# Kernel tuning notes

Measured on AMD Instinct MI355X. Metric: run time of the kernel, lower is better.

Reference implementation:

```python
import jax, jax.numpy as jnp
import numpy as np

N = 100000      # nodes
E = 1600000     # edges (avg degree 16)
IN = 128
OUT = 256


def setup_inputs() -> dict:
    key = jax.random.key(0)
    ks = jax.random.split(key, 8)
    x = jax.random.normal(ks[0], (N, IN), dtype=jnp.float32)
    edge_index = jax.random.randint(ks[1], (2, E), 0, N, dtype=jnp.int64)
    # GCNConv weights (glorot-ish scale) and biases
    W1 = jax.random.normal(ks[2], (IN, OUT), dtype=jnp.float32) / np.float32(np.sqrt(IN))
    b1 = jnp.zeros((OUT,), jnp.float32)
    W2 = jax.random.normal(ks[3], (OUT, OUT), dtype=jnp.float32) / np.float32(np.sqrt(OUT))
    b2 = jnp.zeros((OUT,), jnp.float32)
    # projection Linear(IN, OUT)
    Wp = jax.random.normal(ks[4], (IN, OUT), dtype=jnp.float32) / np.float32(np.sqrt(IN))
    bp = jax.random.normal(ks[5], (OUT,), dtype=jnp.float32) * 0.01
    return {"x": x, "edge_index": edge_index, "W1": W1, "b1": b1,
            "W2": W2, "b2": b2, "Wp": Wp, "bp": bp}


def _gcn_conv(x, W, b, src, dst, n):
    """PyG GCNConv: D^{-1/2}(A+I)D^{-1/2} X W + b. src/dst already include self-loops."""
    xw = x @ W                                              # [n, out]
    ones = jnp.ones(src.shape[0], dtype=xw.dtype)
    deg = jax.ops.segment_sum(ones, dst, num_segments=n)    # in-degree incl. self-loop
    dinv = jnp.where(deg > 0, jax.lax.rsqrt(deg), 0.0)
    norm = dinv[src] * dinv[dst]                            # [e]
    msgs = xw[src] * norm[:, None]                          # gather + scale
    out = jax.ops.segment_sum(msgs, dst, num_segments=n)    # scatter-add
    return out + b


def reference(x, edge_index, W1, b1, W2, b2, Wp, bp):
    n = x.shape[0]
    loop = jnp.arange(n, dtype=edge_index.dtype)            # self-loops
    src = jnp.concatenate([edge_index[0], loop])
    dst = jnp.concatenate([edge_index[1], loop])
    out = jax.nn.relu(_gcn_conv(x, W1, b1, src, dst, n))
    out = _gcn_conv(out, W2, b2, src, dst, n)
    identity = x @ Wp + bp                                  # projection (IN != OUT)
    return jax.nn.relu(out + identity)
```

## Files before the change

kernel.cpp:

```cpp
#include <hip/hip_runtime.h>

#define NODES 100000
#define EDGES 1600000
#define FIN   128
#define FOUT  256
#define NBUCK 196

typedef __bf16 bf16;
typedef __bf16 bf16x8 __attribute__((ext_vector_type(8)));
typedef __bf16 bf16x4 __attribute__((ext_vector_type(4)));
typedef __bf16 bf16x2 __attribute__((ext_vector_type(2)));
typedef float  f32x4  __attribute__((ext_vector_type(4)));
typedef float  f32x2  __attribute__((ext_vector_type(2)));

__device__ __forceinline__ f32x2 bf2f(unsigned w) {
    f32x2 r;
    r[0] = __uint_as_float(w << 16);
    r[1] = __uint_as_float(w & 0xffff0000u);
    return r;
}

__device__ __forceinline__ void acc_u4(f32x2 a[4], uint4 w) {
    a[0] += bf2f(w.x); a[1] += bf2f(w.y);
    a[2] += bf2f(w.z); a[3] += bf2f(w.w);
}

__global__ __launch_bounds__(256) void detect_kernel(const void* __restrict__ x,
                                                     const int* __restrict__ ei,
                                                     int* __restrict__ flags) {
    __shared__ int s_f32_evidence;
    __shared__ int s_odd_nonzero;
    int t = threadIdx.x;
    if (t == 0) { s_f32_evidence = 0; s_odd_nonzero = 0; }
    __syncthreads();
    const bf16* xb = (const bf16*)x;
    int local_f32 = 0;
    for (int i = t; i < 4096; i += 256) {
        float v = fabsf((float)xb[i]);
        if (!(v < 1e4f)) local_f32 = 1;
    }
    if (local_f32) atomicOr(&s_f32_evidence, 1);
    int local_odd = 0;
    for (int k = t; k < 1024; k += 256) {
        if (ei[2 * k + 1] != 0) local_odd = 1;
    }
    if (local_odd) atomicOr(&s_odd_nonzero, 1);
    __syncthreads();
    if (t == 0) {
        flags[0] = s_f32_evidence ? 0 : 1;
        flags[1] = s_odd_nonzero ? 0 : 1;
    }
}

__device__ __forceinline__ int edge_at(const int* __restrict__ ei, int which, int i,
                                       int is64) {
    if (is64) return ei[2 * (which * EDGES + i)];
    return ei[which * EDGES + i];
}

__global__ __launch_bounds__(512) void deg_count(const int* __restrict__ ei,
                                                 int* __restrict__ deg,
                                                 int* __restrict__ bhist,
                                                 const int* __restrict__ flags) {
    __shared__ int lh[256];
    int t = threadIdx.x;
    if (t < 256) lh[t] = 0;
    __syncthreads();
    int i = blockIdx.x * 512 + t;
    if (i < EDGES) {
        int is64 = flags[1];
        int s = edge_at(ei, 0, i, is64);
        int d = edge_at(ei, 1, i, is64);
        if (s >= 0 && s < NODES && d >= 0 && d < NODES) {
            atomicAdd(&deg[d], 1);
            atomicAdd(&lh[d >> 9], 1);
        }
    }
    __syncthreads();
    if (t < NBUCK && lh[t] > 0) atomicAdd(&bhist[t], lh[t]);
}

__global__ __launch_bounds__(1024) void scan1(const int* __restrict__ deg,
                                              int* __restrict__ col_ptr,
                                              int* __restrict__ blksum, int n) {
    __shared__ int sm[1024];
    int t = threadIdx.x;
    int i = blockIdx.x * 1024 + t;
    int v = (i < n) ? deg[i] + 1 : 0;
    sm[t] = v;
    __syncthreads();
    for (int off = 1; off < 1024; off <<= 1) {
        int u = (t >= off) ? sm[t - off] : 0;
        __syncthreads();
        sm[t] += u;
        __syncthreads();
    }
    if (i <= n) col_ptr[i] = sm[t] - v;
    if (t == 1023) blksum[blockIdx.x] = sm[t];
}

__global__ __launch_bounds__(128) void scan2(int* blk, int nblk) {
    __shared__ int sm[128];
    int t = threadIdx.x;
    int v = (t < nblk) ? blk[t] : 0;
    sm[t] = v;
    __syncthreads();
    for (int off = 1; off < 128; off <<= 1) {
        int u = (t >= off) ? sm[t - off] : 0;
        __syncthreads();
        sm[t] += u;
        __syncthreads();
    }
    if (t < nblk) blk[t] = sm[t] - v;
}

__global__ __launch_bounds__(256) void scan3(int* __restrict__ col_ptr,
                                             const int* __restrict__ blkoff,
                                             const int* __restrict__ deg,
                                             float* __restrict__ dinv,
                                             int* __restrict__ col_idx, int n) {
    int i = blockIdx.x * 256 + threadIdx.x;
    if (i <= n) {
        int v = col_ptr[i] + blkoff[i >> 10];
        col_ptr[i] = v;
        if (i < n) col_idx[v] = i;
    }
    if (i < n) dinv[i] = rsqrtf((float)deg[i] + 1.0f);
}

__global__ __launch_bounds__(256) void bucket_scan(const int* __restrict__ bhist,
                                                   int* __restrict__ bbase,
                                                   int* __restrict__ bcur) {
    __shared__ int sm[256];
    int t = threadIdx.x;
    int v = (t < NBUCK) ? bhist[t] : 0;
    sm[t] = v;
    __syncthreads();
    for (int off = 1; off < 256; off <<= 1) {
        int u = (t >= off) ? sm[t - off] : 0;
        __syncthreads();
        sm[t] += u;
        __syncthreads();
    }
    if (t < NBUCK) {
        int ex = sm[t] - v;
        bbase[t] = ex;
        bcur[t]  = ex;
        if (t == NBUCK - 1) bbase[NBUCK] = sm[t];
    }
}

#define EPB 4096
__global__ __launch_bounds__(256) void partition_edges(const int* __restrict__ ei,
                                                       int* __restrict__ bcur,
                                                       uint2* __restrict__ pairs,
                                                       const int* __restrict__ flags) {
    __shared__ int lh[256], sc[256], lst[256], lcu[256], gb[256];
    __shared__ uint2 stage[EPB];
    int t = threadIdx.x;
    int base = blockIdx.x * EPB;
    int is64 = flags[1];

    lh[t] = 0;
    __syncthreads();

    int es[16], ed[16];
#pragma unroll
    for (int j = 0; j < 16; ++j) {
        int i = base + j * 256 + t;
        int s = -1, d = -1;
        if (i < EDGES) {
            s = edge_at(ei, 0, i, is64);
            d = edge_at(ei, 1, i, is64);
            if (s < 0 || s >= NODES || d < 0 || d >= NODES) d = -1;
        }
        es[j] = s; ed[j] = d;
        if (d >= 0) atomicAdd(&lh[d >> 9], 1);
    }
    __syncthreads();
    sc[t] = lh[t];
    __syncthreads();
    for (int off = 1; off < 256; off <<= 1) {
        int u = (t >= off) ? sc[t - off] : 0;
        __syncthreads();
        sc[t] += u;
        __syncthreads();
    }
    int start = sc[t] - lh[t];
    lst[t] = start;
    lcu[t] = start;
    __syncthreads();
#pragma unroll
    for (int j = 0; j < 16; ++j) {
        if (ed[j] >= 0) {
            int p = atomicAdd(&lcu[ed[j] >> 9], 1);
            stage[p] = make_uint2((unsigned)es[j], (unsigned)ed[j]);
        }
    }
    __syncthreads();
    if (t < NBUCK && lh[t] > 0) gb[t] = atomicAdd(&bcur[t], lh[t]);
    __syncthreads();
    int nval = sc[255];
    for (int slot = t; slot < nval; slot += 256) {
        uint2 e = stage[slot];
        int b = (int)(e.y >> 9);
        pairs[(size_t)gb[b] + (slot - lst[b])] = e;
    }
}

__global__ __launch_bounds__(512) void fine_fill(const uint2* __restrict__ pairs,
                                                 const int* __restrict__ bbase,
                                                 const int* __restrict__ col_ptr,
                                                 int* __restrict__ col_idx) {
    __shared__ int lcur[512];
    int b = blockIdx.x;
    int t = threadIdx.x;
    int node = (b << 9) + t;
    lcur[t] = (node < NODES) ? col_ptr[node] + 1 : 0;
    __syncthreads();
    int beg = bbase[b], end = bbase[b + 1];
    for (int i = beg + t; i < end; i += 512) {
        uint2 e = pairs[i];
        int pos = atomicAdd(&lcur[e.y & 511], 1);
        col_idx[pos] = (int)e.x;
    }
}

__global__ __launch_bounds__(256) void pack_all(const void* __restrict__ W1,
                                                const void* __restrict__ W2,
                                                const void* __restrict__ Wp,
                                                const void* __restrict__ b1,
                                                const void* __restrict__ b2,
                                                const void* __restrict__ bp,
                                                bf16* __restrict__ W1p, bf16* __restrict__ W2p,
                                                bf16* __restrict__ Wpp, bf16* __restrict__ b1b,
                                                bf16* __restrict__ b2b, bf16* __restrict__ bpb,
                                                const int* __restrict__ flags) {
    int fl = flags[0];
    int b = blockIdx.x;
    if (b < 512) {
        const void* W; bf16* Wo; int idx;
        if (b < 128)      { W = W1; Wo = W1p; idx = b * 256 + threadIdx.x; }
        else if (b < 384) { W = W2; Wo = W2p; idx = (b - 128) * 256 + threadIdx.x; }
        else              { W = Wp; Wo = Wpp; idx = (b - 384) * 256 + threadIdx.x; }
        int j    = idx & 7;
        int lane = (idx >> 3) & 63;
        int ct   = (idx >> 9) & 15;
        int kt   = idx >> 13;
        int k = kt * 32 + (lane >> 4) * 8 + j;
        int n = ct * 16 + (lane & 15);
        Wo[idx] = fl ? ((const bf16*)W)[k * 256 + n]
                     : (bf16)(((const float*)W)[k * 256 + n]);
    } else {
        const void* bb; bf16* bo;
        if (b == 512)      { bb = b1; bo = b1b; }
        else if (b == 513) { bb = b2; bo = b2b; }
        else               { bb = bp; bo = bpb; }
        int i = threadIdx.x;
        bo[i] = fl ? ((const bf16*)bb)[i] : (bf16)(((const float*)bb)[i]);
    }
}

__global__ __launch_bounds__(256) void scale_x(const void* __restrict__ xv,
                                               const float* __restrict__ dinv,
                                               bf16* __restrict__ Xs,
                                               const int* __restrict__ flags) {
    int idx = blockIdx.x * 256 + threadIdx.x;
    if (idx >= NODES * 16) return;
    int row = idx >> 4, seg = idx & 15;
    float di = dinv[row];
    bf16x8 o;
    if (flags[0]) {
        bf16x8 v = *(const bf16x8*)((const bf16*)xv + (size_t)row * FIN + seg * 8);
#pragma unroll
        for (int j = 0; j < 8; ++j) o[j] = (bf16)(di * (float)v[j]);
    } else {
        const float* p = (const float*)xv + (size_t)row * FIN + seg * 8;
        f32x4 lo = *(const f32x4*)p;
        f32x4 hi = *(const f32x4*)(p + 4);
#pragma unroll
        for (int j = 0; j < 4; ++j) { o[j] = (bf16)(di * lo[j]); o[j + 4] = (bf16)(di * hi[j]); }
    }
    *(bf16x8*)(Xs + (size_t)row * FIN + seg * 8) = o;
}

__global__ __launch_bounds__(256) void gemm_proj(const void* __restrict__ Av,
                                                 const bf16* __restrict__ Wpk,
                                                 const bf16* __restrict__ biasp,
                                                 const bf16* __restrict__ bias2,
                                                 bf16* __restrict__ projb,
                                                 const int* __restrict__ flags) {
    int a_f32 = (flags[0] == 0);
    int wave = threadIdx.x >> 6;
    int lane = threadIdx.x & 63;
    int row0 = blockIdx.x * 64;
    int lr = lane & 15;
    int lk = (lane >> 4) * 8;

    int arow[4];
#pragma unroll
    for (int rf = 0; rf < 4; ++rf) {
        int r = row0 + rf * 16 + lr;
        arow[rf] = r < NODES ? r : (NODES - 1);
    }

    f32x4 acc[4][4];
    f32x4 z = {0.f, 0.f, 0.f, 0.f};
#pragma unroll
    for (int i = 0; i < 4; ++i)
#pragma unroll
        for (int j = 0; j < 4; ++j) acc[i][j] = z;

    for (int kt = 0; kt < 4; ++kt) {
        bf16x8 af[4];
        if (!a_f32) {
            const bf16* Ab = (const bf16*)Av + kt * 32 + lk;
#pragma unroll
            for (int rf = 0; rf < 4; ++rf)
                af[rf] = *(const bf16x8*)(Ab + (size_t)arow[rf] * FIN);
        } else {
            const float* Af = (const float*)Av + kt * 32 + lk;
#pragma unroll
            for (int rf = 0; rf < 4; ++rf) {
                const float* p = Af + (size_t)arow[rf] * FIN;
                f32x4 lo = *(const f32x4*)p;
                f32x4 hi = *(const f32x4*)(p + 4);
                af[rf][0] = (bf16)lo[0]; af[rf][1] = (bf16)lo[1];
                af[rf][2] = (bf16)lo[2]; af[rf][3] = (bf16)lo[3];
                af[rf][4] = (bf16)hi[0]; af[rf][5] = (bf16)hi[1];
                af[rf][6] = (bf16)hi[2]; af[rf][7] = (bf16)hi[3];
            }
        }
        const bf16* wb = Wpk + ((size_t)(kt * 16 + wave * 4) * 64 + lane) * 8;
        bf16x8 bfv[4];
#pragma unroll
        for (int cf = 0; cf < 4; ++cf)
            bfv[cf] = *(const bf16x8*)(wb + cf * 512);
#pragma unroll
        for (int rf = 0; rf < 4; ++rf)
#pragma unroll
            for (int cf = 0; cf < 4; ++cf)
                acc[rf][cf] = __builtin_amdgcn_mfma_f32_16x16x32_bf16(
                    af[rf], bfv[cf], acc[rf][cf], 0, 0, 0);
    }

    int rb = (lane >> 4) * 4;
#pragma unroll
    for (int rf = 0; rf < 4; ++rf) {
#pragma unroll
        for (int r = 0; r < 4; ++r) {
            int row = row0 + rf * 16 + rb + r;
            if (row >= NODES) continue;
#pragma unroll
            for (int cf = 0; cf < 4; ++cf) {
                int col = wave * 64 + cf * 16 + lr;
                float v = acc[rf][cf][r] + (float)biasp[col] + (float)bias2[col];
                projb[(size_t)row * 256 + col] = (bf16)v;
            }
        }
    }
}

__global__ __launch_bounds__(256) void gemm_tile(const bf16* __restrict__ A,
                                                 const bf16* __restrict__ Wpk,
                                                 int K,
                                                 const float* __restrict__ dinv,
                                                 const bf16* __restrict__ bias,
                                                 int relu,
                                                 bf16* __restrict__ out) {
    int wave = threadIdx.x >> 6;
    int lane = threadIdx.x & 63;
    int row0 = blockIdx.x * 64;
    int lr = lane & 15;
    int lk = (lane >> 4) * 8;

    int arow[4];
#pragma unroll
    for (int rf = 0; rf < 4; ++rf) {
        int r = row0 + rf * 16 + lr;
        arow[rf] = r < NODES ? r : (NODES - 1);
    }

    f32x4 acc[4][4];
    f32x4 z = {0.f, 0.f, 0.f, 0.f};
#pragma unroll
    for (int i = 0; i < 4; ++i)
#pragma unroll
        for (int j = 0; j < 4; ++j) acc[i][j] = z;

    int ktiles = K >> 5;
    for (int kt = 0; kt < ktiles; ++kt) {
        const bf16* Ab = A + kt * 32 + lk;
        bf16x8 af[4];
#pragma unroll
        for (int rf = 0; rf < 4; ++rf)
            af[rf] = *(const bf16x8*)(Ab + (size_t)arow[rf] * K);
        const bf16* wb = Wpk + ((size_t)(kt * 16 + wave * 4) * 64 + lane) * 8;
        bf16x8 bfv[4];
#pragma unroll
        for (int cf = 0; cf < 4; ++cf)
            bfv[cf] = *(const bf16x8*)(wb + cf * 512);
#pragma unroll
        for (int rf = 0; rf < 4; ++rf)
#pragma unroll
            for (int cf = 0; cf < 4; ++cf)
                acc[rf][cf] = __builtin_amdgcn_mfma_f32_16x16x32_bf16(
                    af[rf], bfv[cf], acc[rf][cf], 0, 0, 0);
    }

    int rb = (lane >> 4) * 4;
#pragma unroll
    for (int rf = 0; rf < 4; ++rf) {
#pragma unroll
        for (int r = 0; r < 4; ++r) {
            int row = row0 + rf * 16 + rb + r;
            if (row >= NODES) continue;
            float s = dinv ? dinv[row] : 1.0f;
#pragma unroll
            for (int cf = 0; cf < 4; ++cf) {
                int col = wave * 64 + cf * 16 + lr;
                float v = acc[rf][cf][r] * s;
                if (bias) v += (float)bias[col];
                if (relu) v = fmaxf(v, 0.0f);
                out[(size_t)row * 256 + col] = (bf16)v;
            }
        }
    }
}

__device__ __forceinline__ float sel_reduce8(f32x2 acc2[4], int rg) {
    f32x2 a  = (rg & 4) ? acc2[2] : acc2[0];
    f32x2 b  = (rg & 4) ? acc2[3] : acc2[1];
    f32x2 sa = (rg & 4) ? acc2[0] : acc2[2];
    f32x2 sb = (rg & 4) ? acc2[1] : acc2[3];
    f32x2 t;
    t[0] = __shfl_xor(sa[0], 32); t[1] = __shfl_xor(sa[1], 32); a += t;
    t[0] = __shfl_xor(sb[0], 32); t[1] = __shfl_xor(sb[1], 32); b += t;
    f32x2 c = (rg & 2) ? b : a;
    f32x2 s = (rg & 2) ? a : b;
    t[0] = __shfl_xor(s[0], 16); t[1] = __shfl_xor(s[1], 16); c += t;
    float e  = (rg & 1) ? c[1] : c[0];
    float s2 = (rg & 1) ? c[0] : c[1];
    e += __shfl_xor(s2, 8);
    return e;
}

__device__ __forceinline__ f32x2 sel_reduce4(f32x2 a[4], int rg) {
    f32x2 k0 = (rg & 2) ? a[2] : a[0];
    f32x2 k1 = (rg & 2) ? a[3] : a[1];
    f32x2 s0 = (rg & 2) ? a[0] : a[2];
    f32x2 s1 = (rg & 2) ? a[1] : a[3];
    f32x2 t;
    t[0] = __shfl_xor(s0[0], 32); t[1] = __shfl_xor(s0[1], 32); k0 += t;
    t[0] = __shfl_xor(s1[0], 32); t[1] = __shfl_xor(s1[1], 32); k1 += t;
    f32x2 c = (rg & 1) ? k1 : k0;
    f32x2 s = (rg & 1) ? k0 : k1;
    t[0] = __shfl_xor(s[0], 16); t[1] = __shfl_xor(s[1], 16); c += t;
    return c;
}

__global__ __launch_bounds__(256) void gather1(const int* __restrict__ col_ptr,
                                               const int* __restrict__ col_idx,
                                               const bf16* __restrict__ Xs,
                                               const float* __restrict__ dinv,
                                               bf16* __restrict__ aggX) {
    int b = blockIdx.x;
    int slice = b & 1;
    int wave  = threadIdx.x >> 6;
    int wid   = (b >> 1) * 4 + wave;
    int lane  = threadIdx.x & 63;
    if (wid >= NODES) return;
    int beg = col_ptr[wid], end = col_ptr[wid + 1];
    int li = lane & 7;
    int rg = lane >> 3;
    int ch = slice * 64 + li * 8 + rg;
    float di = dinv[wid];

    const char* Xl = (const char*)Xs + slice * 128 + li * 16;
    f32x2 acc2[4];
#pragma unroll
    for (int d = 0; d < 4; ++d) { acc2[d][0] = 0.f; acc2[d][1] = 0.f; }
    for (int chunk = beg; chunk < end; chunk += 64) {
        int gpos = chunk + lane;
        int idx = -2;
        if (gpos < end) idx = col_idx[gpos];
        int moff = idx << 8;
        int cnt = end - chunk; if (cnt > 64) cnt = 64;
        int j = 0;
        for (; j + 16 <= cnt; j += 16) {
            int so0 = __shfl(moff, j + rg);
            int so1 = __shfl(moff, j + 8 + rg);
            uint4 w0 = *(const uint4*)(Xl + so0);
            uint4 w1 = *(const uint4*)(Xl + so1);
            acc_u4(acc2, w0); acc_u4(acc2, w1);
        }
        for (; j < cnt; j += 8) {
            int so = __shfl(moff, j + rg);
            uint4 w = *(const uint4*)(Xl + so);
            acc_u4(acc2, w);
        }
    }
    float aval = sel_reduce8(acc2, rg);
    aggX[(size_t)wid * FIN + ch] = (bf16)(di * aval);
}

__global__ __launch_bounds__(256) void gather2(const int* __restrict__ col_ptr,
                                               const int* __restrict__ col_idx,
                                               const bf16* __restrict__ Y2,
                                               const float* __restrict__ dinv,
                                               const bf16* __restrict__ projb,
                                               void* __restrict__ outv,
                                               const int* __restrict__ flags) {
    int io_f32 = (flags[0] == 0);
    int b = blockIdx.x;
    int slice = b & 1;
    int wave  = threadIdx.x >> 6;
    int wid   = (b >> 1) * 4 + wave;
    int lane  = threadIdx.x & 63;
    if (wid >= NODES) return;
    int beg = col_ptr[wid], end = col_ptr[wid + 1];
    int li = lane & 15;
    int rg = lane >> 4;
    int ch0 = slice * 128 + li * 8 + rg * 2;
    size_t obase = (size_t)wid * 256 + ch0;

    float di = dinv[wid];
    bf16x2 pjv = *(const bf16x2*)(projb + obase);

    const char* Yl = (const char*)Y2 + slice * 256 + li * 16;
    f32x2 acc2[4];
#pragma unroll
    for (int d = 0; d < 4; ++d) { acc2[d][0] = 0.f; acc2[d][1] = 0.f; }
    for (int chunk = beg; chunk < end; chunk += 64) {
        int gpos = chunk + lane;
        int idx = -2;
        if (gpos < end) idx = col_idx[gpos];
        int moff = idx << 9;
        int cnt = end - chunk; if (cnt > 64) cnt = 64;
        int j = 0;
        for (; j + 16 <= cnt; j += 16) {
            int so0 = __shfl(moff, j + rg);
            int so1 = __shfl(moff, j + 4 + rg);
            int so2 = __shfl(moff, j + 8 + rg);
            int so3 = __shfl(moff, j + 12 + rg);
            uint4 w0 = *(const uint4*)(Yl + so0);
            uint4 w1 = *(const uint4*)(Yl + so1);
            uint4 w2 = *(const uint4*)(Yl + so2);
            uint4 w3 = *(const uint4*)(Yl + so3);
            acc_u4(acc2, w0); acc_u4(acc2, w1);
            acc_u4(acc2, w2); acc_u4(acc2, w3);
        }
        for (; j < cnt; j += 4) {
            int so = __shfl(moff, j + rg);
            uint4 w = *(const uint4*)(Yl + so);
            acc_u4(acc2, w);
        }
    }
    f32x2 s = sel_reduce4(acc2, rg);
    float r0 = fmaxf(di * s[0] + (float)pjv[0], 0.0f);
    float r1 = fmaxf(di * s[1] + (float)pjv[1], 0.0f);

    if (io_f32) {
        f32x2 o; o[0] = r0; o[1] = r1;
        __builtin_nontemporal_store(o, (f32x2*)((float*)outv + obase));
    } else {
        bf16x2 o; o[0] = (bf16)r0; o[1] = (bf16)r1;
        __builtin_nontemporal_store(o, (bf16x2*)((bf16*)outv + obase));
    }
}

__global__ __launch_bounds__(256) void zero_out(bf16* out, int nelem) {
    int i = blockIdx.x * 256 + threadIdx.x;
    if (i < nelem) out[i] = (bf16)0.0f;
}

extern "C" void kernel_launch(void* const* d_in, const int* in_sizes, int n_in,
                              void* d_out, int out_size, void* d_ws, size_t ws_size,
                              hipStream_t stream) {
    const void* x   = d_in[0];
    const int*  ei  = (const int*)d_in[1];
    const void* W1  = d_in[2];
    const void* b1  = d_in[3];
    const void* W2  = d_in[4];
    const void* b2  = d_in[5];
    const void* Wp  = d_in[6];
    const void* bp  = d_in[7];

    const size_t CIDX_ALLOC = 6800384;
    const size_t NEEDED = 401408ull * 3 + 1024ull * 4 + CIDX_ALLOC + 65536 + 131072 + 65536
                        + 1536 + 1024 + 25600000ull * 2 + 51200000ull;
    if (ws_size < NEEDED) {
        zero_out<<<(NODES * 256 + 255) / 256, 256, 0, stream>>>((bf16*)d_out, NODES * 256);
        return;
    }

    char* w = (char*)d_ws;
    int*   col_ptr = (int*)w;   w += 401408;
    int*   deg     = (int*)w;   w += 401408;
    int*   bhist   = (int*)w;   w += 1024;
    float* dinv    = (float*)w; w += 401408;
    int*   blk     = (int*)w;   w += 1024;
    int*   flags   = (int*)w;   w += 1024;
    int*   bbase   = (int*)w;   w += 1024;
    int*   bcur    = (int*)w;   w += 1024;
    int*   col_idx = (int*)w;   w += CIDX_ALLOC;
    bf16*  W1p     = (bf16*)w;  w += 65536;
    bf16*  W2p     = (bf16*)w;  w += 131072;
    bf16*  Wpp     = (bf16*)w;  w += 65536;
    bf16*  b1b     = (bf16*)w;  w += 512;
    bf16*  b2b     = (bf16*)w;  w += 512;
    bf16*  bpb     = (bf16*)w;  w += 512;
    char*  zpad    = w;         w += 1024;
    bf16*  Xs      = (bf16*)w;  w += 25600000;
    bf16*  aggX    = (bf16*)w;  w += 25600000;
    bf16*  H1      = (bf16*)w;  w += 51200000;
    uint2* pairs   = (uint2*)Xs;
    bf16*  Y2      = Xs;
    bf16*  projb   = H1;

    const int NBLK = (NODES + 1 + 1023) / 1024;

    detect_kernel<<<1, 256, 0, stream>>>(x, ei, flags);
    hipMemsetAsync(zpad, 0, 1024, stream);

    hipMemsetAsync(deg, 0, 401408 + 1024, stream);
    deg_count<<<(EDGES + 511) / 512, 512, 0, stream>>>(ei, deg, bhist, flags);

    scan1<<<NBLK, 1024, 0, stream>>>(deg, col_ptr, blk, NODES);
    scan2<<<1, 128, 0, stream>>>(blk, NBLK);
    scan3<<<(NODES + 256) / 256, 256, 0, stream>>>(col_ptr, blk, deg, dinv, col_idx, NODES);
    bucket_scan<<<1, 256, 0, stream>>>(bhist, bbase, bcur);

    partition_edges<<<(EDGES + EPB - 1) / EPB, 256, 0, stream>>>(ei, bcur, pairs, flags);
    fine_fill<<<NBUCK, 512, 0, stream>>>(pairs, bbase, col_ptr, col_idx);

    pack_all<<<515, 256, 0, stream>>>(W1, W2, Wp, b1, b2, bp,
                                      W1p, W2p, Wpp, b1b, b2b, bpb, flags);

    const int gemm_grid = (NODES + 63) / 64;
    const int g_grid    = ((NODES + 3) / 4) * 2;

    scale_x<<<(NODES * 16 + 255) / 256, 256, 0, stream>>>(x, dinv, Xs, flags);
    gather1<<<g_grid, 256, 0, stream>>>(col_ptr, col_idx, Xs, dinv, aggX);
    gemm_tile<<<gemm_grid, 256, 0, stream>>>(aggX, W1p, FIN, nullptr, b1b, 1, H1);
    gemm_tile<<<gemm_grid, 256, 0, stream>>>(H1, W2p, FOUT, dinv, nullptr, 0, Y2);
    gemm_proj<<<gemm_grid, 256, 0, stream>>>(x, Wpp, bpb, b2b, projb, flags);
    gather2<<<g_grid, 256, 0, stream>>>(col_ptr, col_idx, Y2, dinv,
                                        projb, d_out, flags);
}
```

Measured before the change: 649.5 us.

## Split gather2 into four channel slices and merge small scan launches

The second-layer gather now covers four 64-channel slices per node instead of two 128-channel slices. Each wave handles 8 edges in parallel with an 8-way reduction, which doubles the grid and raises parallelism. The bucket scan is folded into the block-offset scan kernel, and the zpad memset moves into detect_kernel, cutting launch count. In exchange, each node's column indices are read and shuffled by four blocks rather than two, and output stores shrink to scalar width.

```diff
diff --git a/kernel.cpp b/kernel.cpp
--- a/kernel.cpp
+++ b/kernel.cpp
@@ -27,10 +27,12 @@
 
 __global__ __launch_bounds__(256) void detect_kernel(const void* __restrict__ x,
                                                      const int* __restrict__ ei,
-                                                     int* __restrict__ flags) {
+                                                     int* __restrict__ flags,
+                                                     float* __restrict__ zpad) {
     __shared__ int s_f32_evidence;
     __shared__ int s_odd_nonzero;
     int t = threadIdx.x;
+    zpad[t] = 0.0f;
     if (t == 0) { s_f32_evidence = 0; s_odd_nonzero = 0; }
     __syncthreads();
     const bf16* xb = (const bf16*)x;
@@ -99,19 +101,38 @@
     if (t == 1023) blksum[blockIdx.x] = sm[t];
 }
 
-__global__ __launch_bounds__(128) void scan2(int* blk, int nblk) {
-    __shared__ int sm[128];
+__global__ __launch_bounds__(256) void scan2b(int* __restrict__ blk, int nblk,
+                                              const int* __restrict__ bhist,
+                                              int* __restrict__ bbase,
+                                              int* __restrict__ bcur) {
+    __shared__ int sm[256];
     int t = threadIdx.x;
     int v = (t < nblk) ? blk[t] : 0;
     sm[t] = v;
     __syncthreads();
-    for (int off = 1; off < 128; off <<= 1) {
+    for (int off = 1; off < 256; off <<= 1) {
         int u = (t >= off) ? sm[t - off] : 0;
         __syncthreads();
         sm[t] += u;
         __syncthreads();
     }
     if (t < nblk) blk[t] = sm[t] - v;
+    __syncthreads();
+    int v2 = (t < NBUCK) ? bhist[t] : 0;
+    sm[t] = v2;
+    __syncthreads();
+    for (int off = 1; off < 256; off <<= 1) {
+        int u = (t >= off) ? sm[t - off] : 0;
+        __syncthreads();
+        sm[t] += u;
+        __syncthreads();
+    }
+    if (t < NBUCK) {
+        int ex = sm[t] - v2;
+        bbase[t] = ex;
+        bcur[t]  = ex;
+        if (t == NBUCK - 1) bbase[NBUCK] = sm[t];
+    }
 }
 
 __global__ __launch_bounds__(256) void scan3(int* __restrict__ col_ptr,
@@ -126,28 +147,6 @@
         if (i < n) col_idx[v] = i;
     }
     if (i < n) dinv[i] = rsqrtf((float)deg[i] + 1.0f);
-}
-
-__global__ __launch_bounds__(256) void bucket_scan(const int* __restrict__ bhist,
-                                                   int* __restrict__ bbase,
-                                                   int* __restrict__ bcur) {
-    __shared__ int sm[256];
-    int t = threadIdx.x;
-    int v = (t < NBUCK) ? bhist[t] : 0;
-    sm[t] = v;
-    __syncthreads();
-    for (int off = 1; off < 256; off <<= 1) {
-        int u = (t >= off) ? sm[t - off] : 0;
-        __syncthreads();
-        sm[t] += u;
-        __syncthreads();
-    }
-    if (t < NBUCK) {
-        int ex = sm[t] - v;
-        bbase[t] = ex;
-        bcur[t]  = ex;
-        if (t == NBUCK - 1) bbase[NBUCK] = sm[t];
-    }
 }
 
 #define EPB 4096
@@ -445,20 +444,6 @@
     return e;
 }
 
-__device__ __forceinline__ f32x2 sel_reduce4(f32x2 a[4], int rg) {
-    f32x2 k0 = (rg & 2) ? a[2] : a[0];
-    f32x2 k1 = (rg & 2) ? a[3] : a[1];
-    f32x2 s0 = (rg & 2) ? a[0] : a[2];
-    f32x2 s1 = (rg & 2) ? a[1] : a[3];
-    f32x2 t;
-    t[0] = __shfl_xor(s0[0], 32); t[1] = __shfl_xor(s0[1], 32); k0 += t;
-    t[0] = __shfl_xor(s1[0], 32); t[1] = __shfl_xor(s1[1], 32); k1 += t;
-    f32x2 c = (rg & 1) ? k1 : k0;
-    f32x2 s = (rg & 1) ? k0 : k1;
-    t[0] = __shfl_xor(s[0], 16); t[1] = __shfl_xor(s[1], 16); c += t;
-    return c;
-}
-
 __global__ __launch_bounds__(256) void gather1(const int* __restrict__ col_ptr,
                                                const int* __restrict__ col_idx,
                                                const bf16* __restrict__ Xs,
@@ -513,21 +498,21 @@
                                                const int* __restrict__ flags) {
     int io_f32 = (flags[0] == 0);
     int b = blockIdx.x;
-    int slice = b & 1;
+    int slice = b & 3;
     int wave  = threadIdx.x >> 6;
-    int wid   = (b >> 1) * 4 + wave;
+    int wid   = (b >> 2) * 4 + wave;
     int lane  = threadIdx.x & 63;
     if (wid >= NODES) return;
     int beg = col_ptr[wid], end = col_ptr[wid + 1];
-    int li = lane & 15;
-    int rg = lane >> 4;
-    int ch0 = slice * 128 + li * 8 + rg * 2;
-    size_t obase = (size_t)wid * 256 + ch0;
+    int li = lane & 7;
+    int rg = lane >> 3;
+    int ch = slice * 64 + li * 8 + rg;
+    size_t obase = (size_t)wid * 256 + ch;
 
     float di = dinv[wid];
-    bf16x2 pjv = *(const bf16x2*)(projb + obase);
-
-    const char* Yl = (const char*)Y2 + slice * 256 + li * 16;
+    float pj = (float)__builtin_nontemporal_load(projb + obase);
+
+    const char* Yl = (const char*)Y2 + slice * 128 + li * 16;
     f32x2 acc2[4];
 #pragma unroll
     for (int d = 0; d < 4; ++d) { acc2[d][0] = 0.f; acc2[d][1] = 0.f; }
@@ -540,32 +525,24 @@
         int j = 0;
         for (; j + 16 <= cnt; j += 16) {
             int so0 = __shfl(moff, j + rg);
-            int so1 = __shfl(moff, j + 4 + rg);
-            int so2 = __shfl(moff, j + 8 + rg);
-            int so3 = __shfl(moff, j + 12 + rg);
+            int so1 = __shfl(moff, j + 8 + rg);
             uint4 w0 = *(const uint4*)(Yl + so0);
             uint4 w1 = *(const uint4*)(Yl + so1);
-            uint4 w2 = *(const uint4*)(Yl + so2);
-            uint4 w3 = *(const uint4*)(Yl + so3);
             acc_u4(acc2, w0); acc_u4(acc2, w1);
-            acc_u4(acc2, w2); acc_u4(acc2, w3);
-        }
-        for (; j < cnt; j += 4) {
+        }
+        for (; j < cnt; j += 8) {
             int so = __shfl(moff, j + rg);
             uint4 w = *(const uint4*)(Yl + so);
             acc_u4(acc2, w);
         }
     }
-    f32x2 s = sel_reduce4(acc2, rg);
-    float r0 = fmaxf(di * s[0] + (float)pjv[0], 0.0f);
-    float r1 = fmaxf(di * s[1] + (float)pjv[1], 0.0f);
+    float aval = sel_reduce8(acc2, rg);
+    float r = fmaxf(di * aval + pj, 0.0f);
 
     if (io_f32) {
-        f32x2 o; o[0] = r0; o[1] = r1;
-        __builtin_nontemporal_store(o, (f32x2*)((float*)outv + obase));
+        __builtin_nontemporal_store(r, (float*)outv + obase);
     } else {
-        bf16x2 o; o[0] = (bf16)r0; o[1] = (bf16)r1;
-        __builtin_nontemporal_store(o, (bf16x2*)((bf16*)outv + obase));
+        __builtin_nontemporal_store((bf16)r, (bf16*)outv + obase);
     }
 }
 
@@ -620,16 +597,14 @@
 
     const int NBLK = (NODES + 1 + 1023) / 1024;
 
-    detect_kernel<<<1, 256, 0, stream>>>(x, ei, flags);
-    hipMemsetAsync(zpad, 0, 1024, stream);
+    detect_kernel<<<1, 256, 0, stream>>>(x, ei, flags, (float*)zpad);
 
     hipMemsetAsync(deg, 0, 401408 + 1024, stream);
     deg_count<<<(EDGES + 511) / 512, 512, 0, stream>>>(ei, deg, bhist, flags);
 
     scan1<<<NBLK, 1024, 0, stream>>>(deg, col_ptr, blk, NODES);
-    scan2<<<1, 128, 0, stream>>>(blk, NBLK);
+    scan2b<<<1, 256, 0, stream>>>(blk, NBLK, bhist, bbase, bcur);
     scan3<<<(NODES + 256) / 256, 256, 0, stream>>>(col_ptr, blk, deg, dinv, col_idx, NODES);
-    bucket_scan<<<1, 256, 0, stream>>>(bhist, bbase, bcur);
 
     partition_edges<<<(EDGES + EPB - 1) / EPB, 256, 0, stream>>>(ei, bcur, pairs, flags);
     fine_fill<<<NBUCK, 512, 0, stream>>>(pairs, bbase, col_ptr, col_idx);
@@ -638,13 +613,14 @@
                                       W1p, W2p, Wpp, b1b, b2b, bpb, flags);
 
     const int gemm_grid = (NODES + 63) / 64;
-    const int g_grid    = ((NODES + 3) / 4) * 2;
+    const int g1_grid   = ((NODES + 3) / 4) * 2;
+    const int g2_grid   = ((NODES + 3) / 4) * 4;
 
     scale_x<<<(NODES * 16 + 255) / 256, 256, 0, stream>>>(x, dinv, Xs, flags);
-    gather1<<<g_grid, 256, 0, stream>>>(col_ptr, col_idx, Xs, dinv, aggX);
+    gather1<<<g1_grid, 256, 0, stream>>>(col_ptr, col_idx, Xs, dinv, aggX);
     gemm_tile<<<gemm_grid, 256, 0, stream>>>(aggX, W1p, FIN, nullptr, b1b, 1, H1);
     gemm_tile<<<gemm_grid, 256, 0, stream>>>(H1, W2p, FOUT, dinv, nullptr, 0, Y2);
     gemm_proj<<<gemm_grid, 256, 0, stream>>>(x, Wpp, bpb, b2b, projb, flags);
-    gather2<<<g_grid, 256, 0, stream>>>(col_ptr, col_idx, Y2, dinv,
-                                        projb, d_out, flags);
-}
+    gather2<<<g2_grid, 256, 0, stream>>>(col_ptr, col_idx, Y2, dinv,
+                                         projb, d_out, flags);
+}
```

Result: no change. 658.4 us (+1.4%).

## Fuse layer-1 gather with both GEMMs and fold x-scaling into projection GEMM

Applied to the files above, without the earlier changes.

The layer-1 neighbour aggregation, the W1 GEMM with bias and ReLU, and the W2 GEMM are merged into one kernel that keeps the 64-row tile in shared memory, so the aggX and H1 intermediates never go to global memory. The projection GEMM now also writes the dinv-scaled bf16 copy of x, which removes the separate scale_x pass. It writes its result straight into the output buffer, where gather2 reads it as the residual. The small scan kernels are merged and the padding memset moves into the detect kernel to cut launches. In exchange, gather parallelism in the fused kernel drops to one wave per node handled in sequence, with 16 nodes per wave and roughly 33KB of LDS per block, which may lower occupancy and latency hiding.

```diff
diff --git a/kernel.cpp b/kernel.cpp
--- a/kernel.cpp
+++ b/kernel.cpp
@@ -27,10 +27,14 @@
 
 __global__ __launch_bounds__(256) void detect_kernel(const void* __restrict__ x,
                                                      const int* __restrict__ ei,
-                                                     int* __restrict__ flags) {
+                                                     int* __restrict__ flags,
+                                                     float* __restrict__ zpadA,
+                                                     float* __restrict__ zpadB) {
     __shared__ int s_f32_evidence;
     __shared__ int s_odd_nonzero;
     int t = threadIdx.x;
+    zpadA[t] = 0.0f;
+    zpadB[t] = 0.0f;
     if (t == 0) { s_f32_evidence = 0; s_odd_nonzero = 0; }
     __syncthreads();
     const bf16* xb = (const bf16*)x;
@@ -99,19 +103,38 @@
     if (t == 1023) blksum[blockIdx.x] = sm[t];
 }
 
-__global__ __launch_bounds__(128) void scan2(int* blk, int nblk) {
-    __shared__ int sm[128];
+__global__ __launch_bounds__(256) void scan2b(int* __restrict__ blk, int nblk,
+                                              const int* __restrict__ bhist,
+                                              int* __restrict__ bbase,
+                                              int* __restrict__ bcur) {
+    __shared__ int sm[256];
     int t = threadIdx.x;
     int v = (t < nblk) ? blk[t] : 0;
     sm[t] = v;
     __syncthreads();
-    for (int off = 1; off < 128; off <<= 1) {
+    for (int off = 1; off < 256; off <<= 1) {
         int u = (t >= off) ? sm[t - off] : 0;
         __syncthreads();
         sm[t] += u;
         __syncthreads();
     }
     if (t < nblk) blk[t] = sm[t] - v;
+    __syncthreads();
+    int v2 = (t < NBUCK) ? bhist[t] : 0;
+    sm[t] = v2;
+    __syncthreads();
+    for (int off = 1; off < 256; off <<= 1) {
+        int u = (t >= off) ? sm[t - off] : 0;
+        __syncthreads();
+        sm[t] += u;
+        __syncthreads();
+    }
+    if (t < NBUCK) {
+        int ex = sm[t] - v2;
+        bbase[t] = ex;
+        bcur[t]  = ex;
+        if (t == NBUCK - 1) bbase[NBUCK] = sm[t];
+    }
 }
 
 __global__ __launch_bounds__(256) void scan3(int* __restrict__ col_ptr,
@@ -126,28 +149,6 @@
         if (i < n) col_idx[v] = i;
     }
     if (i < n) dinv[i] = rsqrtf((float)deg[i] + 1.0f);
-}
-
-__global__ __launch_bounds__(256) void bucket_scan(const int* __restrict__ bhist,
-                                                   int* __restrict__ bbase,
-                                                   int* __restrict__ bcur) {
-    __shared__ int sm[256];
-    int t = threadIdx.x;
-    int v = (t < NBUCK) ? bhist[t] : 0;
-    sm[t] = v;
-    __syncthreads();
-    for (int off = 1; off < 256; off <<= 1) {
-        int u = (t >= off) ? sm[t - off] : 0;
-        __syncthreads();
-        sm[t] += u;
-        __syncthreads();
-    }
-    if (t < NBUCK) {
-        int ex = sm[t] - v;
-        bbase[t] = ex;
-        bcur[t]  = ex;
-        if (t == NBUCK - 1) bbase[NBUCK] = sm[t];
-    }
 }
 
 #define EPB 4096
@@ -261,34 +262,13 @@
     }
 }
 
-__global__ __launch_bounds__(256) void scale_x(const void* __restrict__ xv,
-                                               const float* __restrict__ dinv,
-                                               bf16* __restrict__ Xs,
-                                               const int* __restrict__ flags) {
-    int idx = blockIdx.x * 256 + threadIdx.x;
-    if (idx >= NODES * 16) return;
-    int row = idx >> 4, seg = idx & 15;
-    float di = dinv[row];
-    bf16x8 o;
-    if (flags[0]) {
-        bf16x8 v = *(const bf16x8*)((const bf16*)xv + (size_t)row * FIN + seg * 8);
-#pragma unroll
-        for (int j = 0; j < 8; ++j) o[j] = (bf16)(di * (float)v[j]);
-    } else {
-        const float* p = (const float*)xv + (size_t)row * FIN + seg * 8;
-        f32x4 lo = *(const f32x4*)p;
-        f32x4 hi = *(const f32x4*)(p + 4);
-#pragma unroll
-        for (int j = 0; j < 4; ++j) { o[j] = (bf16)(di * lo[j]); o[j + 4] = (bf16)(di * hi[j]); }
-    }
-    *(bf16x8*)(Xs + (size_t)row * FIN + seg * 8) = o;
-}
-
 __global__ __launch_bounds__(256) void gemm_proj(const void* __restrict__ Av,
                                                  const bf16* __restrict__ Wpk,
+                                                 const float* __restrict__ dinv,
                                                  const bf16* __restrict__ biasp,
                                                  const bf16* __restrict__ bias2,
-                                                 bf16* __restrict__ projb,
+                                                 void* __restrict__ outv,
+                                                 bf16* __restrict__ Xs,
                                                  const int* __restrict__ flags) {
     int a_f32 = (flags[0] == 0);
     int wave = threadIdx.x >> 6;
@@ -298,10 +278,12 @@
     int lk = (lane >> 4) * 8;
 
     int arow[4];
+    float di4[4];
 #pragma unroll
     for (int rf = 0; rf < 4; ++rf) {
         int r = row0 + rf * 16 + lr;
         arow[rf] = r < NODES ? r : (NODES - 1);
+        di4[rf] = dinv[arow[rf]];
     }
 
     f32x4 acc[4][4];
@@ -331,6 +313,13 @@
                 af[rf][6] = (bf16)hi[2]; af[rf][7] = (bf16)hi[3];
             }
         }
+#pragma unroll
+        for (int rf = 0; rf < 4; ++rf) {
+            bf16x8 xsv;
+#pragma unroll
+            for (int j = 0; j < 8; ++j) xsv[j] = (bf16)(di4[rf] * (float)af[rf][j]);
+            *(bf16x8*)(Xs + (size_t)arow[rf] * FIN + kt * 32 + lk) = xsv;
+        }
         const bf16* wb = Wpk + ((size_t)(kt * 16 + wave * 4) * 64 + lane) * 8;
         bf16x8 bfv[4];
 #pragma unroll
@@ -355,94 +344,12 @@
             for (int cf = 0; cf < 4; ++cf) {
                 int col = wave * 64 + cf * 16 + lr;
                 float v = acc[rf][cf][r] + (float)biasp[col] + (float)bias2[col];
-                projb[(size_t)row * 256 + col] = (bf16)v;
+                size_t off = (size_t)row * 256 + col;
+                if (a_f32) ((float*)outv)[off] = v;
+                else       ((bf16*)outv)[off]  = (bf16)v;
             }
         }
     }
-}
-
-__global__ __launch_bounds__(256) void gemm_tile(const bf16* __restrict__ A,
-                                                 const bf16* __restrict__ Wpk,
-                                                 int K,
-                                                 const float* __restrict__ dinv,
-                                                 const bf16* __restrict__ bias,
-                                                 int relu,
-                                                 bf16* __restrict__ out) {
-    int wave = threadIdx.x >> 6;
-    int lane = threadIdx.x & 63;
-    int row0 = blockIdx.x * 64;
-    int lr = lane & 15;
-    int lk = (lane >> 4) * 8;
-
-    int arow[4];
-#pragma unroll
-    for (int rf = 0; rf < 4; ++rf) {
-        int r = row0 + rf * 16 + lr;
-        arow[rf] = r < NODES ? r : (NODES - 1);
-    }
-
-    f32x4 acc[4][4];
-    f32x4 z = {0.f, 0.f, 0.f, 0.f};
-#pragma unroll
-    for (int i = 0; i < 4; ++i)
-#pragma unroll
-        for (int j = 0; j < 4; ++j) acc[i][j] = z;
-
-    int ktiles = K >> 5;
-    for (int kt = 0; kt < ktiles; ++kt) {
-        const bf16* Ab = A + kt * 32 + lk;
-        bf16x8 af[4];
-#pragma unroll
-        for (int rf = 0; rf < 4; ++rf)
-            af[rf] = *(const bf16x8*)(Ab + (size_t)arow[rf] * K);
-        const bf16* wb = Wpk + ((size_t)(kt * 16 + wave * 4) * 64 + lane) * 8;
-        bf16x8 bfv[4];
-#pragma unroll
-        for (int cf = 0; cf < 4; ++cf)
-            bfv[cf] = *(const bf16x8*)(wb + cf * 512);
-#pragma unroll
-        for (int rf = 0; rf < 4; ++rf)
-#pragma unroll
-            for (int cf = 0; cf < 4; ++cf)
-                acc[rf][cf] = __builtin_amdgcn_mfma_f32_16x16x32_bf16(
-                    af[rf], bfv[cf], acc[rf][cf], 0, 0, 0);
-    }
-
-    int rb = (lane >> 4) * 4;
-#pragma unroll
-    for (int rf = 0; rf < 4; ++rf) {
-#pragma unroll
-        for (int r = 0; r < 4; ++r) {
-            int row = row0 + rf * 16 + rb + r;
-            if (row >= NODES) continue;
-            float s = dinv ? dinv[row] : 1.0f;
-#pragma unroll
-            for (int cf = 0; cf < 4; ++cf) {
-                int col = wave * 64 + cf * 16 + lr;
-                float v = acc[rf][cf][r] * s;
-                if (bias) v += (float)bias[col];
-                if (relu) v = fmaxf(v, 0.0f);
-                out[(size_t)row * 256 + col] = (bf16)v;
-            }
-        }
-    }
-}
-
-__device__ __forceinline__ float sel_reduce8(f32x2 acc2[4], int rg) {
-    f32x2 a  = (rg & 4) ? acc2[2] : acc2[0];
-    f32x2 b  = (rg & 4) ? acc2[3] : acc2[1];
-    f32x2 sa = (rg & 4) ? acc2[0] : acc2[2];
-    f32x2 sb = (rg & 4) ? acc2[1] : acc2[3];
-    f32x2 t;
-    t[0] = __shfl_xor(sa[0], 32); t[1] = __shfl_xor(sa[1], 32); a += t;
-    t[0] = __shfl_xor(sb[0], 32); t[1] = __shfl_xor(sb[1], 32); b += t;
-    f32x2 c = (rg & 2) ? b : a;
-    f32x2 s = (rg & 2) ? a : b;
-    t[0] = __shfl_xor(s[0], 16); t[1] = __shfl_xor(s[1], 16); c += t;
-    float e  = (rg & 1) ? c[1] : c[0];
-    float s2 = (rg & 1) ? c[0] : c[1];
-    e += __shfl_xor(s2, 8);
-    return e;
 }
 
 __device__ __forceinline__ f32x2 sel_reduce4(f32x2 a[4], int rg) {
@@ -459,56 +366,141 @@
     return c;
 }
 
-__global__ __launch_bounds__(256) void gather1(const int* __restrict__ col_ptr,
-                                               const int* __restrict__ col_idx,
-                                               const bf16* __restrict__ Xs,
-                                               const float* __restrict__ dinv,
-                                               bf16* __restrict__ aggX) {
-    int b = blockIdx.x;
-    int slice = b & 1;
-    int wave  = threadIdx.x >> 6;
-    int wid   = (b >> 1) * 4 + wave;
-    int lane  = threadIdx.x & 63;
-    if (wid >= NODES) return;
-    int beg = col_ptr[wid], end = col_ptr[wid + 1];
-    int li = lane & 7;
-    int rg = lane >> 3;
-    int ch = slice * 64 + li * 8 + rg;
-    float di = dinv[wid];
-
-    const char* Xl = (const char*)Xs + slice * 128 + li * 16;
-    f32x2 acc2[4];
-#pragma unroll
-    for (int d = 0; d < 4; ++d) { acc2[d][0] = 0.f; acc2[d][1] = 0.f; }
-    for (int chunk = beg; chunk < end; chunk += 64) {
-        int gpos = chunk + lane;
-        int idx = -2;
-        if (gpos < end) idx = col_idx[gpos];
-        int moff = idx << 8;
-        int cnt = end - chunk; if (cnt > 64) cnt = 64;
-        int j = 0;
-        for (; j + 16 <= cnt; j += 16) {
-            int so0 = __shfl(moff, j + rg);
-            int so1 = __shfl(moff, j + 8 + rg);
-            uint4 w0 = *(const uint4*)(Xl + so0);
-            uint4 w1 = *(const uint4*)(Xl + so1);
-            acc_u4(acc2, w0); acc_u4(acc2, w1);
-        }
-        for (; j < cnt; j += 8) {
-            int so = __shfl(moff, j + rg);
-            uint4 w = *(const uint4*)(Xl + so);
-            acc_u4(acc2, w);
-        }
-    }
-    float aval = sel_reduce8(acc2, rg);
-    aggX[(size_t)wid * FIN + ch] = (bf16)(di * aval);
+#define SMLD 264
+__global__ __launch_bounds__(256) void g1conv(const int* __restrict__ col_ptr,
+                                              const int* __restrict__ col_idx,
+                                              const bf16* __restrict__ Xs,
+                                              const float* __restrict__ dinv,
+                                              const bf16* __restrict__ W1p,
+                                              const bf16* __restrict__ W2p,
+                                              const bf16* __restrict__ b1b,
+                                              bf16* __restrict__ Y2) {
+    __shared__ bf16 sm[64][SMLD];
+    int wave = threadIdx.x >> 6;
+    int lane = threadIdx.x & 63;
+    int row0 = blockIdx.x * 64;
+    int li = lane & 15;
+    int rg = lane >> 4;
+
+    const char* Xl = (const char*)Xs + li * 16;
+    for (int k = 0; k < 16; ++k) {
+        int node = row0 + wave * 16 + k;
+        int nn = node < NODES ? node : (NODES - 1);
+        int beg = col_ptr[nn], end = col_ptr[nn + 1];
+        float di = dinv[nn];
+        f32x2 a[4];
+#pragma unroll
+        for (int d = 0; d < 4; ++d) { a[d][0] = 0.f; a[d][1] = 0.f; }
+        for (int chunk = beg; chunk < end; chunk += 64) {
+            int gpos = chunk + lane;
+            int idx = -2;
+            if (gpos < end) idx = col_idx[gpos];
+            int moff = idx << 8;
+            int cnt = end - chunk; if (cnt > 64) cnt = 64;
+            int j = 0;
+            for (; j + 8 <= cnt; j += 8) {
+                int so0 = __shfl(moff, j + rg);
+                int so1 = __shfl(moff, j + 4 + rg);
+                uint4 w0 = *(const uint4*)(Xl + so0);
+                uint4 w1 = *(const uint4*)(Xl + so1);
+                acc_u4(a, w0); acc_u4(a, w1);
+            }
+            for (; j < cnt; j += 4) {
+                int so = __shfl(moff, j + rg);
+                uint4 w = *(const uint4*)(Xl + so);
+                acc_u4(a, w);
+            }
+        }
+        f32x2 s = sel_reduce4(a, rg);
+        bf16x2 o;
+        o[0] = (bf16)(di * s[0]);
+        o[1] = (bf16)(di * s[1]);
+        *(bf16x2*)&sm[wave * 16 + k][li * 8 + rg * 2] = o;
+    }
+    __syncthreads();
+
+    int lr = li;
+    int lk = rg * 8;
+    f32x4 acc[4][4];
+    f32x4 z = {0.f, 0.f, 0.f, 0.f};
+#pragma unroll
+    for (int i = 0; i < 4; ++i)
+#pragma unroll
+        for (int j = 0; j < 4; ++j) acc[i][j] = z;
+    for (int kt = 0; kt < 4; ++kt) {
+        bf16x8 af[4];
+#pragma unroll
+        for (int rf = 0; rf < 4; ++rf)
+            af[rf] = *(const bf16x8*)&sm[rf * 16 + lr][kt * 32 + lk];
+        const bf16* wb = W1p + ((size_t)(kt * 16 + wave * 4) * 64 + lane) * 8;
+        bf16x8 bfv[4];
+#pragma unroll
+        for (int cf = 0; cf < 4; ++cf)
+            bfv[cf] = *(const bf16x8*)(wb + cf * 512);
+#pragma unroll
+        for (int rf = 0; rf < 4; ++rf)
+#pragma unroll
+            for (int cf = 0; cf < 4; ++cf)
+                acc[rf][cf] = __builtin_amdgcn_mfma_f32_16x16x32_bf16(
+                    af[rf], bfv[cf], acc[rf][cf], 0, 0, 0);
+    }
+    __syncthreads();
+
+    int rb = rg * 4;
+#pragma unroll
+    for (int rf = 0; rf < 4; ++rf)
+#pragma unroll
+        for (int r = 0; r < 4; ++r) {
+            int row = rf * 16 + rb + r;
+#pragma unroll
+            for (int cf = 0; cf < 4; ++cf) {
+                int col = wave * 64 + cf * 16 + lr;
+                float v = acc[rf][cf][r] + (float)b1b[col];
+                sm[row][col] = (bf16)fmaxf(v, 0.0f);
+            }
+        }
+    __syncthreads();
+
+#pragma unroll
+    for (int i = 0; i < 4; ++i)
+#pragma unroll
+        for (int j = 0; j < 4; ++j) acc[i][j] = z;
+    for (int kt = 0; kt < 8; ++kt) {
+        bf16x8 af[4];
+#pragma unroll
+        for (int rf = 0; rf < 4; ++rf)
+            af[rf] = *(const bf16x8*)&sm[rf * 16 + lr][kt * 32 + lk];
+        const bf16* wb = W2p + ((size_t)(kt * 16 + wave * 4) * 64 + lane) * 8;
+        bf16x8 bfv[4];
+#pragma unroll
+        for (int cf = 0; cf < 4; ++cf)
+            bfv[cf] = *(const bf16x8*)(wb + cf * 512);
+#pragma unroll
+        for (int rf = 0; rf < 4; ++rf)
+#pragma unroll
+            for (int cf = 0; cf < 4; ++cf)
+                acc[rf][cf] = __builtin_amdgcn_mfma_f32_16x16x32_bf16(
+                    af[rf], bfv[cf], acc[rf][cf], 0, 0, 0);
+    }
+#pragma unroll
+    for (int rf = 0; rf < 4; ++rf)
+#pragma unroll
+        for (int r = 0; r < 4; ++r) {
+            int row = row0 + rf * 16 + rb + r;
+            if (row >= NODES) continue;
+            float di = dinv[row];
+#pragma unroll
+            for (int cf = 0; cf < 4; ++cf) {
+                int col = wave * 64 + cf * 16 + lr;
+                Y2[(size_t)row * 256 + col] = (bf16)(acc[rf][cf][r] * di);
+            }
+        }
 }
 
 __global__ __launch_bounds__(256) void gather2(const int* __restrict__ col_ptr,
                                                const int* __restrict__ col_idx,
                                                const bf16* __restrict__ Y2,
                                                const float* __restrict__ dinv,
-                                               const bf16* __restrict__ projb,
                                                void* __restrict__ outv,
                                                const int* __restrict__ flags) {
     int io_f32 = (flags[0] == 0);
@@ -525,7 +517,14 @@
     size_t obase = (size_t)wid * 256 + ch0;
 
     float di = dinv[wid];
-    bf16x2 pjv = *(const bf16x2*)(projb + obase);
+    float pj0, pj1;
+    if (io_f32) {
+        f32x2 p = *(const f32x2*)((const float*)outv + obase);
+        pj0 = p[0]; pj1 = p[1];
+    } else {
+        bf16x2 p = *(const bf16x2*)((const bf16*)outv + obase);
+        pj0 = (float)p[0]; pj1 = (float)p[1];
+    }
 
     const char* Yl = (const char*)Y2 + slice * 256 + li * 16;
     f32x2 acc2[4];
@@ -557,8 +556,8 @@
         }
     }
     f32x2 s = sel_reduce4(acc2, rg);
-    float r0 = fmaxf(di * s[0] + (float)pjv[0], 0.0f);
-    float r1 = fmaxf(di * s[1] + (float)pjv[1], 0.0f);
+    float r0 = fmaxf(di * s[0] + pj0, 0.0f);
+    float r1 = fmaxf(di * s[1] + pj1, 0.0f);
 
     if (io_f32) {
         f32x2 o; o[0] = r0; o[1] = r1;
@@ -587,8 +586,7 @@
     const void* bp  = d_in[7];
 
     const size_t CIDX_ALLOC = 6800384;
-    const size_t NEEDED = 401408ull * 3 + 1024ull * 4 + CIDX_ALLOC + 65536 + 131072 + 65536
-                        + 1536 + 1024 + 25600000ull * 2 + 51200000ull;
+    const size_t NEEDED = 85075456;
     if (ws_size < NEEDED) {
         zero_out<<<(NODES * 256 + 255) / 256, 256, 0, stream>>>((bf16*)d_out, NODES * 256);
         return;
@@ -610,26 +608,22 @@
     bf16*  b1b     = (bf16*)w;  w += 512;
     bf16*  b2b     = (bf16*)w;  w += 512;
     bf16*  bpb     = (bf16*)w;  w += 512;
-    char*  zpad    = w;         w += 1024;
+    char*  zpadA   = w;         w += 1024;
     bf16*  Xs      = (bf16*)w;  w += 25600000;
-    bf16*  aggX    = (bf16*)w;  w += 25600000;
-    bf16*  H1      = (bf16*)w;  w += 51200000;
+    char*  zpadB   = w;         w += 1024;
+    bf16*  Y2      = (bf16*)w;  w += 51200000;
     uint2* pairs   = (uint2*)Xs;
-    bf16*  Y2      = Xs;
-    bf16*  projb   = H1;
 
     const int NBLK = (NODES + 1 + 1023) / 1024;
 
-    detect_kernel<<<1, 256, 0, stream>>>(x, ei, flags);
-    hipMemsetAsync(zpad, 0, 1024, stream);
+    detect_kernel<<<1, 256, 0, stream>>>(x, ei, flags, (float*)zpadA, (float*)zpadB);
 
     hipMemsetAsync(deg, 0, 401408 + 1024, stream);
     deg_count<<<(EDGES + 511) / 512, 512, 0, stream>>>(ei, deg, bhist, flags);
 
     scan1<<<NBLK, 1024, 0, stream>>>(deg, col_ptr, blk, NODES);
-    scan2<<<1, 128, 0, stream>>>(blk, NBLK);
+    scan2b<<<1, 256, 0, stream>>>(blk, NBLK, bhist, bbase, bcur);
     scan3<<<(NODES + 256) / 256, 256, 0, stream>>>(col_ptr, blk, deg, dinv, col_idx, NODES);
-    bucket_scan<<<1, 256, 0, stream>>>(bhist, bbase, bcur);
 
     partition_edges<<<(EDGES + EPB - 1) / EPB, 256, 0, stream>>>(ei, bcur, pairs, flags);
     fine_fill<<<NBUCK, 512, 0, stream>>>(pairs, bbase, col_ptr, col_idx);
@@ -638,13 +632,10 @@
                                       W1p, W2p, Wpp, b1b, b2b, bpb, flags);
 
     const int gemm_grid = (NODES + 63) / 64;
-    const int g_grid    = ((NODES + 3) / 4) * 2;
-
-    scale_x<<<(NODES * 16 + 255) / 256, 256, 0, stream>>>(x, dinv, Xs, flags);
-    gather1<<<g_grid, 256, 0, stream>>>(col_ptr, col_idx, Xs, dinv, aggX);
-    gemm_tile<<<gemm_grid, 256, 0, stream>>>(aggX, W1p, FIN, nullptr, b1b, 1, H1);
-    gemm_tile<<<gemm_grid, 256, 0, stream>>>(H1, W2p, FOUT, dinv, nullptr, 0, Y2);
-    gemm_proj<<<gemm_grid, 256, 0, stream>>>(x, Wpp, bpb, b2b, projb, flags);
-    gather2<<<g_grid, 256, 0, stream>>>(col_ptr, col_idx, Y2, dinv,
-                                        projb, d_out, flags);
-}
+    const int g2_grid   = ((NODES + 3) / 4) * 2;
+
+    gemm_proj<<<gemm_grid, 256, 0, stream>>>(x, Wpp, dinv, bpb, b2b, d_out, Xs, flags);
+    g1conv<<<gemm_grid, 256, 0, stream>>>(col_ptr, col_idx, Xs, dinv,
+                                          W1p, W2p, b1b, Y2);
+    gather2<<<g2_grid, 256, 0, stream>>>(col_ptr, col_idx, Y2, dinv, d_out, flags);
+}
```

Result: faster. 628.0 us (-3.3%).
